# Kernel optimization log

Measured on AMD Instinct MI355X. Metric: run time of the kernel, lower is better.

Reference implementation:

```python
import jax, jax.numpy as jnp
import numpy as np

H = 64            # hidden_size
HORIZON = 168     # forecast_horizon = 7*24


def lstm_cell(x, h, c, Wih, Whh, bih, bhh):
    # PyTorch LSTM gate order: i, f, g, o
    g = x @ Wih.T + bih + h @ Whh.T + bhh          # [B, 4H]
    i, f, gg, o = jnp.split(g, 4, axis=-1)
    i = jax.nn.sigmoid(i)
    f = jax.nn.sigmoid(f)
    gg = jnp.tanh(gg)
    o = jax.nn.sigmoid(o)
    c_new = f * c + i * gg
    h_new = o * jnp.tanh(c_new)
    return h_new, c_new


def run_layer(xs, Wih, Whh, bih, bhh):
    # xs: [T, B, in] -> (hs [T, B, H], h_final, c_final), zero initial state
    B = xs.shape[1]
    h0 = jnp.zeros((B, H), xs.dtype)
    c0 = jnp.zeros((B, H), xs.dtype)

    def step(carry, x_t):
        h, c = carry
        h, c = lstm_cell(x_t, h, c, Wih, Whh, bih, bhh)
        return (h, c), h

    (hf, cf), hs = jax.lax.scan(step, (h0, c0), xs)
    return hs, hf, cf


def setup_inputs() -> dict:
    key = jax.random.key(0)
    ks = iter(jax.random.split(key, 32))
    B, T, IN = 8192, 336, 1
    bound = 1.0 / np.sqrt(H)  # PyTorch default LSTM init scale

    def u(shape):
        return jax.random.uniform(next(ks), shape, jnp.float32, -bound, bound)

    def lstm_params(in_dim):
        return u((4 * H, in_dim)), u((4 * H, H)), u((4 * H,)), u((4 * H,))

    enc_Wih0, enc_Whh0, enc_bih0, enc_bhh0 = lstm_params(IN)
    enc_Wih1, enc_Whh1, enc_bih1, enc_bhh1 = lstm_params(H)
    dec_Wih0, dec_Whh0, dec_bih0, dec_bhh0 = lstm_params(H)
    dec_Wih1, dec_Whh1, dec_bih1, dec_bhh1 = lstm_params(H)
    fc_W = u((1, H))
    fc_b = u((1,))

    x = jax.random.normal(next(ks), (B, T, IN), jnp.float32)
    return dict(
        x=x,
        enc_Wih0=enc_Wih0, enc_Whh0=enc_Whh0, enc_bih0=enc_bih0, enc_bhh0=enc_bhh0,
        enc_Wih1=enc_Wih1, enc_Whh1=enc_Whh1, enc_bih1=enc_bih1, enc_bhh1=enc_bhh1,
        dec_Wih0=dec_Wih0, dec_Whh0=dec_Whh0, dec_bih0=dec_bih0, dec_bhh0=dec_bhh0,
        dec_Wih1=dec_Wih1, dec_Whh1=dec_Whh1, dec_bih1=dec_bih1, dec_bhh1=dec_bhh1,
        fc_W=fc_W, fc_b=fc_b,
    )


def reference(x,
              enc_Wih0, enc_Whh0, enc_bih0, enc_bhh0,
              enc_Wih1, enc_Whh1, enc_bih1, enc_bhh1,
              dec_Wih0, dec_Whh0, dec_bih0, dec_bhh0,
              dec_Wih1, dec_Whh1, dec_bih1, dec_bhh1,
              fc_W, fc_b):
    B = x.shape[0]
    xs = jnp.swapaxes(x, 0, 1)                      # [T, B, 1]

    # Encoder: 2-layer LSTM, keep final (h, c) per layer
    hs0, h0f, c0f = run_layer(xs, enc_Wih0, enc_Whh0, enc_bih0, enc_bhh0)
    _, h1f, c1f = run_layer(hs0, enc_Wih1, enc_Whh1, enc_bih1, enc_bhh1)

    dec_in0 = jnp.zeros((B, H), x.dtype)

    def dstep(carry, _):
        h0, c0, h1, c1, xin = carry
        h0, c0 = lstm_cell(xin, h0, c0, dec_Wih0, dec_Whh0, dec_bih0, dec_bhh0)
        h1, c1 = lstm_cell(h0, h1, c1, dec_Wih1, dec_Whh1, dec_bih1, dec_bhh1)
        pred = h1 @ fc_W.T + fc_b                   # [B, 1]
        return (h0, c0, h1, c1, h1), pred

    _, preds = jax.lax.scan(dstep, (h0f, c0f, h1f, c1f, dec_in0), None, length=HORIZON)
    return jnp.swapaxes(preds, 0, 1)                # [B, 168, 1]
```

## Files before the change

kernel.cpp:

```cpp
#include <hip/hip_runtime.h>


#define TT  336
#define HZN 168
#define NT  512
#define ROWS 16
#define XP  340

typedef short s8v __attribute__((ext_vector_type(8)));
typedef short s2v __attribute__((ext_vector_type(2)));
typedef float f4v __attribute__((ext_vector_type(4)));

__device__ __forceinline__ float fexp(float v){
  return __builtin_amdgcn_exp2f(v * 1.44269504088896340736f);
}
__device__ __forceinline__ float sigm(float v){
  return __builtin_amdgcn_rcpf(1.0f + fexp(-v));
}
__device__ __forceinline__ float tanh_(float v){
  return 1.0f - 2.0f * __builtin_amdgcn_rcpf(1.0f + fexp(2.0f * v));
}

__device__ __forceinline__ short bf16rne(float f){
  unsigned u = __float_as_uint(f);
  return (short)((u + 0x7fffu + ((u >> 16) & 1u)) >> 16);
}

__device__ __forceinline__ s8v ldH(const short* hb, int l, int kt){
  int b  = l & 15;
  int gr = kt*4 + (l >> 4);
  return *(const s8v*)(hb + b*64 + ((gr ^ (b & 7)) << 3));
}

__device__ __forceinline__ s8v ldW(const float* __restrict__ Wm, int w, int l,
                                   int mt, int kt){
  int mm   = l & 15;
  int grow = (mm & 3)*64 + w*8 + 2*(mm >> 2) + mt;
  int k0   = kt*32 + (l >> 4)*8;
  const float* p = Wm + grow*64 + k0;
  float4 q0 = *(const float4*)(p);
  float4 q1 = *(const float4*)(p + 4);
  s8v v;
  v[0]=bf16rne(q0.x); v[1]=bf16rne(q0.y); v[2]=bf16rne(q0.z); v[3]=bf16rne(q0.w);
  v[4]=bf16rne(q1.x); v[5]=bf16rne(q1.y); v[6]=bf16rne(q1.z); v[7]=bf16rne(q1.w);
  return v;
}

__device__ __forceinline__ float pwise(f4v a, float& c){
  float I = sigm(a[0]), F = sigm(a[1]), G = tanh_(a[2]), O = sigm(a[3]);
  c = fmaf(F, c, I*G);
  return O * tanh_(c);
}

__device__ __forceinline__ void stH(short* hb, int b, int c0, float hA, float hB){
  int idx = b*64 + (((c0 >> 3) ^ (b & 7)) << 3) + (c0 & 7);
  *(s2v*)(hb + idx) = s2v{bf16rne(hA), bf16rne(hB)};
}

__global__ __launch_bounds__(NT, 4)
void edlstm_kernel(const float* __restrict__ x,
  const float* __restrict__ eWih0, const float* __restrict__ eWhh0,
  const float* __restrict__ ebih0, const float* __restrict__ ebhh0,
  const float* __restrict__ eWih1, const float* __restrict__ eWhh1,
  const float* __restrict__ ebih1, const float* __restrict__ ebhh1,
  const float* __restrict__ dWih0, const float* __restrict__ dWhh0,
  const float* __restrict__ dbih0, const float* __restrict__ dbhh0,
  const float* __restrict__ dWih1, const float* __restrict__ dWhh1,
  const float* __restrict__ dbih1, const float* __restrict__ dbhh1,
  const float* __restrict__ fcW, const float* __restrict__ fcb,
  float* __restrict__ out)
{
  __shared__ float xs[ROWS*XP];
  __shared__ short hS[8192];
  __shared__ float fcred[16*9];
  __shared__ float bE0L[256], bE1L[256], bD0L[256], bD1L[256], wxL[256];

  const int tid = threadIdx.x;
  const int l   = tid & 63;
  const int w   = tid >> 6;
  const int b   = l & 15;
  const int c0  = w*8 + 2*(l >> 4);
  const int brow0 = blockIdx.x * ROWS;

  {
    int4* hz = (int4*)hS;
    #pragma unroll
    for (int k=0; k<2; k++) hz[k*NT + tid] = int4{0,0,0,0};
  }
  #pragma unroll
  for (int k=0; k<3; k++){
    int idx = k*NT + tid;
    if (idx < ROWS*84){
      int row = idx / 84;
      int c   = idx - row*84;
      *(float4*)(xs + row*XP + c*4) =
        *(const float4*)(x + (size_t)(brow0+row)*TT + c*4);
    }
  }
  if (tid < 256){
    int c = tid >> 2, g = tid & 3;
    int j = g*64 + c;
    bE0L[tid] = ebih0[j] + ebhh0[j];
    bE1L[tid] = ebih1[j] + ebhh1[j];
    bD0L[tid] = dbih0[j] + dbhh0[j];
    bD1L[tid] = dbih1[j] + dbhh1[j];
    wxL[tid]  = eWih0[j];
  }

  s8v Whh0[2][2], Wih1[2][2], Whh1[2][2];
  #pragma unroll
  for (int mt=0; mt<2; mt++)
    #pragma unroll
    for (int kt=0; kt<2; kt++){
      Whh0[mt][kt] = ldW(eWhh0, w, l, mt, kt);
      Wih1[mt][kt] = ldW(eWih1, w, l, mt, kt);
      Whh1[mt][kt] = ldW(eWhh1, w, l, mt, kt);
    }

  float cL0a = 0.f, cL0b = 0.f, cL1a = 0.f, cL1b = 0.f;
  int p = 0;
  __syncthreads();

  for (int t=0; t<TT; t++){
    short* h0R = hS        + p*2048;
    short* h0W = hS        + (p^1)*2048;
    short* h1R = hS + 4096 + p*2048;
    short* h1W = hS + 4096 + (p^1)*2048;

    float xv = xs[b*XP + t];
    f4v wxa = *(const f4v*)(wxL + c0*4);
    f4v wxb = *(const f4v*)(wxL + c0*4 + 4);
    f4v aA  = *(const f4v*)(bE0L + c0*4)     + wxa*xv;
    f4v aB  = *(const f4v*)(bE0L + c0*4 + 4) + wxb*xv;
    #pragma unroll
    for (int kt=0; kt<2; kt++){
      s8v hh = ldH(h0R, l, kt);
      aA = __builtin_amdgcn_mfma_f32_16x16x32_bf16(Whh0[0][kt], hh, aA, 0, 0, 0);
      aB = __builtin_amdgcn_mfma_f32_16x16x32_bf16(Whh0[1][kt], hh, aB, 0, 0, 0);
    }
    float h0a = pwise(aA, cL0a);
    float h0b = pwise(aB, cL0b);
    stH(h0W, b, c0, h0a, h0b);
    __syncthreads();

    aA = *(const f4v*)(bE1L + c0*4);
    aB = *(const f4v*)(bE1L + c0*4 + 4);
    #pragma unroll
    for (int kt=0; kt<2; kt++){
      s8v g0 = ldH(h0W, l, kt);
      s8v g1 = ldH(h1R, l, kt);
      aA = __builtin_amdgcn_mfma_f32_16x16x32_bf16(Wih1[0][kt], g0, aA, 0, 0, 0);
      aB = __builtin_amdgcn_mfma_f32_16x16x32_bf16(Wih1[1][kt], g0, aB, 0, 0, 0);
      aA = __builtin_amdgcn_mfma_f32_16x16x32_bf16(Whh1[0][kt], g1, aA, 0, 0, 0);
      aB = __builtin_amdgcn_mfma_f32_16x16x32_bf16(Whh1[1][kt], g1, aB, 0, 0, 0);
    }
    float h1a = pwise(aA, cL1a);
    float h1b = pwise(aB, cL1b);
    stH(h1W, b, c0, h1a, h1b);
    __syncthreads();
    p ^= 1;
  }

  s8v Dih0[2][2];
  #pragma unroll
  for (int mt=0; mt<2; mt++)
    #pragma unroll
    for (int kt=0; kt<2; kt++){
      Dih0[mt][kt] = ldW(dWih0, w, l, mt, kt);
      Whh0[mt][kt] = ldW(dWhh0, w, l, mt, kt);
      Wih1[mt][kt] = ldW(dWih1, w, l, mt, kt);
      Whh1[mt][kt] = ldW(dWhh1, w, l, mt, kt);
    }
  const float fcwA = fcW[c0], fcwB = fcW[c0+1], fcb0 = fcb[0];

  for (int s=0; s<HZN; s++){
    short* h0R = hS        + p*2048;
    short* h0W = hS        + (p^1)*2048;
    short* h1R = hS + 4096 + p*2048;
    short* h1W = hS + 4096 + (p^1)*2048;

    f4v aA = *(const f4v*)(bD0L + c0*4);
    f4v aB = *(const f4v*)(bD0L + c0*4 + 4);
    #pragma unroll
    for (int kt=0; kt<2; kt++){
      s8v hh = ldH(h0R, l, kt);
      aA = __builtin_amdgcn_mfma_f32_16x16x32_bf16(Whh0[0][kt], hh, aA, 0, 0, 0);
      aB = __builtin_amdgcn_mfma_f32_16x16x32_bf16(Whh0[1][kt], hh, aB, 0, 0, 0);
    }
    if (s > 0){
      #pragma unroll
      for (int kt=0; kt<2; kt++){
        s8v hh = ldH(h1R, l, kt);
        aA = __builtin_amdgcn_mfma_f32_16x16x32_bf16(Dih0[0][kt], hh, aA, 0, 0, 0);
        aB = __builtin_amdgcn_mfma_f32_16x16x32_bf16(Dih0[1][kt], hh, aB, 0, 0, 0);
      }
    }
    float h0a = pwise(aA, cL0a);
    float h0b = pwise(aB, cL0b);
    stH(h0W, b, c0, h0a, h0b);
    __syncthreads();

    aA = *(const f4v*)(bD1L + c0*4);
    aB = *(const f4v*)(bD1L + c0*4 + 4);
    #pragma unroll
    for (int kt=0; kt<2; kt++){
      s8v g0 = ldH(h0W, l, kt);
      s8v g1 = ldH(h1R, l, kt);
      aA = __builtin_amdgcn_mfma_f32_16x16x32_bf16(Wih1[0][kt], g0, aA, 0, 0, 0);
      aB = __builtin_amdgcn_mfma_f32_16x16x32_bf16(Wih1[1][kt], g0, aB, 0, 0, 0);
      aA = __builtin_amdgcn_mfma_f32_16x16x32_bf16(Whh1[0][kt], g1, aA, 0, 0, 0);
      aB = __builtin_amdgcn_mfma_f32_16x16x32_bf16(Whh1[1][kt], g1, aB, 0, 0, 0);
    }
    float h1a = pwise(aA, cL1a);
    float h1b = pwise(aB, cL1b);
    stH(h1W, b, c0, h1a, h1b);

    float pr = h1a*fcwA + h1b*fcwB;
    pr += __shfl_xor(pr, 16);
    pr += __shfl_xor(pr, 32);
    if (l < 16) fcred[l*9 + w] = pr;
    __syncthreads();

    if (tid < 16){
      float sm = fcb0;
      #pragma unroll
      for (int j=0; j<8; j++) sm += fcred[tid*9 + j];
      out[(size_t)(brow0 + tid)*HZN + s] = sm;
    }
    p ^= 1;
  }
}

extern "C" void kernel_launch(void* const* d_in, const int* in_sizes, int n_in,
                              void* d_out, int out_size, void* d_ws, size_t ws_size,
                              hipStream_t stream)
{
  (void)in_sizes; (void)n_in; (void)d_ws; (void)ws_size; (void)out_size;
  const float* x     = (const float*)d_in[0];
  const float* eWih0 = (const float*)d_in[1];
  const float* eWhh0 = (const float*)d_in[2];
  const float* ebih0 = (const float*)d_in[3];
  const float* ebhh0 = (const float*)d_in[4];
  const float* eWih1 = (const float*)d_in[5];
  const float* eWhh1 = (const float*)d_in[6];
  const float* ebih1 = (const float*)d_in[7];
  const float* ebhh1 = (const float*)d_in[8];
  const float* dWih0 = (const float*)d_in[9];
  const float* dWhh0 = (const float*)d_in[10];
  const float* dbih0 = (const float*)d_in[11];
  const float* dbhh0 = (const float*)d_in[12];
  const float* dWih1 = (const float*)d_in[13];
  const float* dWhh1 = (const float*)d_in[14];
  const float* dbih1 = (const float*)d_in[15];
  const float* dbhh1 = (const float*)d_in[16];
  const float* fcW   = (const float*)d_in[17];
  const float* fcb   = (const float*)d_in[18];
  float* out = (float*)d_out;

  edlstm_kernel<<<dim3(512), dim3(NT), 0, stream>>>(
      x, eWih0, eWhh0, ebih0, ebhh0, eWih1, eWhh1, ebih1, ebhh1,
      dWih0, dWhh0, dbih0, dbhh0, dWih1, dWhh1, dbih1, dbhh1,
      fcW, fcb, out);
}
```

Measured before the change: 788.1 us.

## Skew encoder layers so layer-0 and layer-1 steps share one barrier

The encoder loop is software-pipelined: each superstep computes layer-1 at time t and layer-0 at time t+1 from the same h0 buffer. This halves the __syncthreads count in the encoder and lets the MFMA chains of both layers interleave. It adds a prologue and epilogue, and both encoder and decoder loops are unrolled by two so buffer parity is static. The decoder logic is unchanged apart from the macro unrolling and swapped buffer indexing.

Result: no change. 772.7 us (-2.0%).

```diff
diff --git a/kernel.cpp b/kernel.cpp
--- a/kernel.cpp
+++ b/kernel.cpp
@@ -11,6 +11,8 @@
 typedef short s2v __attribute__((ext_vector_type(2)));
 typedef float f4v __attribute__((ext_vector_type(4)));
 
+#define MF(wf, hf, c) __builtin_amdgcn_mfma_f32_16x16x32_bf16((wf), (hf), (c), 0, 0, 0)
+
 __device__ __forceinline__ float fexp(float v){
   return __builtin_amdgcn_exp2f(v * 1.44269504088896340736f);
 }
@@ -20,7 +22,6 @@
 __device__ __forceinline__ float tanh_(float v){
   return 1.0f - 2.0f * __builtin_amdgcn_rcpf(1.0f + fexp(2.0f * v));
 }
-
 __device__ __forceinline__ short bf16rne(float f){
   unsigned u = __float_as_uint(f);
   return (short)((u + 0x7fffu + ((u >> 16) & 1u)) >> 16);
@@ -55,6 +56,80 @@
 __device__ __forceinline__ void stH(short* hb, int b, int c0, float hA, float hB){
   int idx = b*64 + (((c0 >> 3) ^ (b & 7)) << 3) + (c0 & 7);
   *(s2v*)(hb + idx) = s2v{bf16rne(hA), bf16rne(hB)};
+}
+
+#define ENC_SUPER(P, t, DO_L0) {                                            \
+  const short* h0R = hS + (P)*2048;                                         \
+  short*       h0Wr = hS + ((P)^1)*2048;                                    \
+  const short* h1R = hS + 4096 + (P)*2048;                                  \
+  short*       h1Wr = hS + 4096 + ((P)^1)*2048;                             \
+  s8v g00 = ldH(h0R, l, 0), g01 = ldH(h0R, l, 1);                           \
+  s8v g10 = ldH(h1R, l, 0), g11 = ldH(h1R, l, 1);                           \
+  f4v aA = *(const f4v*)(bE1L + c0*4);                                      \
+  f4v aB = *(const f4v*)(bE1L + c0*4 + 4);                                  \
+  f4v aC, aD;                                                               \
+  if (DO_L0){                                                               \
+    float xv = xs[b*XP + (t) + 1];                                          \
+    f4v wxa = *(const f4v*)(wxL + c0*4);                                    \
+    f4v wxb = *(const f4v*)(wxL + c0*4 + 4);                                \
+    aC = *(const f4v*)(bE0L + c0*4)     + wxa*xv;                           \
+    aD = *(const f4v*)(bE0L + c0*4 + 4) + wxb*xv;                           \
+  }                                                                         \
+  aA = MF(Wih1[0][0], g00, aA); aB = MF(Wih1[1][0], g00, aB);               \
+  aA = MF(Wih1[0][1], g01, aA); aB = MF(Wih1[1][1], g01, aB);               \
+  aA = MF(Whh1[0][0], g10, aA); aB = MF(Whh1[1][0], g10, aB);               \
+  aA = MF(Whh1[0][1], g11, aA); aB = MF(Whh1[1][1], g11, aB);               \
+  if (DO_L0){                                                               \
+    aC = MF(Whh0[0][0], g00, aC); aD = MF(Whh0[1][0], g00, aD);             \
+    aC = MF(Whh0[0][1], g01, aC); aD = MF(Whh0[1][1], g01, aD);             \
+  }                                                                         \
+  float h1a = pwise(aA, cL1a), h1b = pwise(aB, cL1b);                       \
+  stH(h1Wr, b, c0, h1a, h1b);                                               \
+  if (DO_L0){                                                               \
+    float h0a = pwise(aC, cL0a), h0b = pwise(aD, cL0b);                     \
+    stH(h0Wr, b, c0, h0a, h0b);                                             \
+  }                                                                         \
+  __syncthreads();                                                          \
+}
+
+#define DEC_STEP(Q, s) {                                                    \
+  const short* h0R = hS + (Q)*2048;                                         \
+  short*       h0Wr = hS + ((Q)^1)*2048;                                    \
+  const short* h1R = hS + 4096 + ((Q)^1)*2048;                              \
+  short*       h1Wr = hS + 4096 + (Q)*2048;                                 \
+  f4v aA = *(const f4v*)(bD0L + c0*4);                                      \
+  f4v aB = *(const f4v*)(bD0L + c0*4 + 4);                                  \
+  s8v f0 = ldH(h0R, l, 0), f1 = ldH(h0R, l, 1);                             \
+  aA = MF(Whh0[0][0], f0, aA); aB = MF(Whh0[1][0], f0, aB);                 \
+  aA = MF(Whh0[0][1], f1, aA); aB = MF(Whh0[1][1], f1, aB);                 \
+  if ((s) > 0){                                                             \
+    s8v e0 = ldH(h1R, l, 0), e1 = ldH(h1R, l, 1);                           \
+    aA = MF(Dih0[0][0], e0, aA); aB = MF(Dih0[1][0], e0, aB);               \
+    aA = MF(Dih0[0][1], e1, aA); aB = MF(Dih0[1][1], e1, aB);               \
+  }                                                                         \
+  float h0a = pwise(aA, cL0a), h0b = pwise(aB, cL0b);                       \
+  stH(h0Wr, b, c0, h0a, h0b);                                               \
+  __syncthreads();                                                          \
+  aA = *(const f4v*)(bD1L + c0*4);                                          \
+  aB = *(const f4v*)(bD1L + c0*4 + 4);                                      \
+  s8v g0 = ldH(h0Wr, l, 0), g1 = ldH(h0Wr, l, 1);                           \
+  s8v e0 = ldH(h1R, l, 0),  e1 = ldH(h1R, l, 1);                            \
+  aA = MF(Wih1[0][0], g0, aA); aB = MF(Wih1[1][0], g0, aB);                 \
+  aA = MF(Wih1[0][1], g1, aA); aB = MF(Wih1[1][1], g1, aB);                 \
+  aA = MF(Whh1[0][0], e0, aA); aB = MF(Whh1[1][0], e0, aB);                 \
+  aA = MF(Whh1[0][1], e1, aA); aB = MF(Whh1[1][1], e1, aB);                 \
+  float h1a = pwise(aA, cL1a), h1b = pwise(aB, cL1b);                       \
+  stH(h1Wr, b, c0, h1a, h1b);                                               \
+  float pr = h1a*fcwA + h1b*fcwB;                                           \
+  pr += __shfl_xor(pr, 16); pr += __shfl_xor(pr, 32);                       \
+  if (l < 16) fcred[l*9 + w] = pr;                                          \
+  __syncthreads();                                                          \
+  if (tid < 16){                                                            \
+    float sm2 = fcb0;                                                       \
+    _Pragma("unroll")                                                       \
+    for (int j=0; j<8; j++) sm2 += fcred[tid*9 + j];                        \
+    out[(size_t)(brow0 + tid)*HZN + (s)] = sm2;                             \
+  }                                                                         \
 }
 
 __global__ __launch_bounds__(NT, 4)
@@ -118,48 +193,25 @@
     }
 
   float cL0a = 0.f, cL0b = 0.f, cL1a = 0.f, cL1b = 0.f;
-  int p = 0;
   __syncthreads();
 
-  for (int t=0; t<TT; t++){
-    short* h0R = hS        + p*2048;
-    short* h0W = hS        + (p^1)*2048;
-    short* h1R = hS + 4096 + p*2048;
-    short* h1W = hS + 4096 + (p^1)*2048;
-
-    float xv = xs[b*XP + t];
+  {
+    float xv = xs[b*XP];
     f4v wxa = *(const f4v*)(wxL + c0*4);
     f4v wxb = *(const f4v*)(wxL + c0*4 + 4);
     f4v aA  = *(const f4v*)(bE0L + c0*4)     + wxa*xv;
     f4v aB  = *(const f4v*)(bE0L + c0*4 + 4) + wxb*xv;
-    #pragma unroll
-    for (int kt=0; kt<2; kt++){
-      s8v hh = ldH(h0R, l, kt);
-      aA = __builtin_amdgcn_mfma_f32_16x16x32_bf16(Whh0[0][kt], hh, aA, 0, 0, 0);
-      aB = __builtin_amdgcn_mfma_f32_16x16x32_bf16(Whh0[1][kt], hh, aB, 0, 0, 0);
-    }
-    float h0a = pwise(aA, cL0a);
-    float h0b = pwise(aB, cL0b);
-    stH(h0W, b, c0, h0a, h0b);
+    float h0a = pwise(aA, cL0a), h0b = pwise(aB, cL0b);
+    stH(hS + 2048, b, c0, h0a, h0b);
     __syncthreads();
-
-    aA = *(const f4v*)(bE1L + c0*4);
-    aB = *(const f4v*)(bE1L + c0*4 + 4);
-    #pragma unroll
-    for (int kt=0; kt<2; kt++){
-      s8v g0 = ldH(h0W, l, kt);
-      s8v g1 = ldH(h1R, l, kt);
-      aA = __builtin_amdgcn_mfma_f32_16x16x32_bf16(Wih1[0][kt], g0, aA, 0, 0, 0);
-      aB = __builtin_amdgcn_mfma_f32_16x16x32_bf16(Wih1[1][kt], g0, aB, 0, 0, 0);
-      aA = __builtin_amdgcn_mfma_f32_16x16x32_bf16(Whh1[0][kt], g1, aA, 0, 0, 0);
-      aB = __builtin_amdgcn_mfma_f32_16x16x32_bf16(Whh1[1][kt], g1, aB, 0, 0, 0);
-    }
-    float h1a = pwise(aA, cL1a);
-    float h1b = pwise(aB, cL1b);
-    stH(h1W, b, c0, h1a, h1b);
-    __syncthreads();
-    p ^= 1;
-  }
+  }
+
+  for (int k=0; k<167; k++){
+    ENC_SUPER(1, 2*k,   1);
+    ENC_SUPER(0, 2*k+1, 1);
+  }
+  ENC_SUPER(1, 334, 1);
+  ENC_SUPER(0, 335, 0);
 
   s8v Dih0[2][2];
   #pragma unroll
@@ -173,61 +225,9 @@
     }
   const float fcwA = fcW[c0], fcwB = fcW[c0+1], fcb0 = fcb[0];
 
-  for (int s=0; s<HZN; s++){
-    short* h0R = hS        + p*2048;
-    short* h0W = hS        + (p^1)*2048;
-    short* h1R = hS + 4096 + p*2048;
-    short* h1W = hS + 4096 + (p^1)*2048;
-
-    f4v aA = *(const f4v*)(bD0L + c0*4);
-    f4v aB = *(const f4v*)(bD0L + c0*4 + 4);
-    #pragma unroll
-    for (int kt=0; kt<2; kt++){
-      s8v hh = ldH(h0R, l, kt);
-      aA = __builtin_amdgcn_mfma_f32_16x16x32_bf16(Whh0[0][kt], hh, aA, 0, 0, 0);
-      aB = __builtin_amdgcn_mfma_f32_16x16x32_bf16(Whh0[1][kt], hh, aB, 0, 0, 0);
-    }
-    if (s > 0){
-      #pragma unroll
-      for (int kt=0; kt<2; kt++){
-        s8v hh = ldH(h1R, l, kt);
-        aA = __builtin_amdgcn_mfma_f32_16x16x32_bf16(Dih0[0][kt], hh, aA, 0, 0, 0);
-        aB = __builtin_amdgcn_mfma_f32_16x16x32_bf16(Dih0[1][kt], hh, aB, 0, 0, 0);
-      }
-    }
-    float h0a = pwise(aA, cL0a);
-    float h0b = pwise(aB, cL0b);
-    stH(h0W, b, c0, h0a, h0b);
-    __syncthreads();
-
-    aA = *(const f4v*)(bD1L + c0*4);
-    aB = *(const f4v*)(bD1L + c0*4 + 4);
-    #pragma unroll
-    for (int kt=0; kt<2; kt++){
-      s8v g0 = ldH(h0W, l, kt);
-      s8v g1 = ldH(h1R, l, kt);
-      aA = __builtin_amdgcn_mfma_f32_16x16x32_bf16(Wih1[0][kt], g0, aA, 0, 0, 0);
-      aB = __builtin_amdgcn_mfma_f32_16x16x32_bf16(Wih1[1][kt], g0, aB, 0, 0, 0);
-      aA = __builtin_amdgcn_mfma_f32_16x16x32_bf16(Whh1[0][kt], g1, aA, 0, 0, 0);
-      aB = __builtin_amdgcn_mfma_f32_16x16x32_bf16(Whh1[1][kt], g1, aB, 0, 0, 0);
-    }
-    float h1a = pwise(aA, cL1a);
-    float h1b = pwise(aB, cL1b);
-    stH(h1W, b, c0, h1a, h1b);
-
-    float pr = h1a*fcwA + h1b*fcwB;
-    pr += __shfl_xor(pr, 16);
-    pr += __shfl_xor(pr, 32);
-    if (l < 16) fcred[l*9 + w] = pr;
-    __syncthreads();
-
-    if (tid < 16){
-      float sm = fcb0;
-      #pragma unroll
-      for (int j=0; j<8; j++) sm += fcred[tid*9 + j];
-      out[(size_t)(brow0 + tid)*HZN + s] = sm;
-    }
-    p ^= 1;
+  for (int k=0; k<84; k++){
+    DEC_STEP(0, 2*k);
+    DEC_STEP(1, 2*k+1);
   }
 }
 
```
